# Kernel tuning notes

Hardware: AMD Instinct MI355X
Metric: run time of the kernel (lower is better)

## Reference

```python
import jax, jax.numpy as jnp
import numpy as np

BN_EPS = 1e-5

def conv_block(x, w, b, g, beta, m, v, a):
    # 1x1 conv (pointwise) + eval-mode BatchNorm2d + PReLU (single shared alpha)
    y = jnp.einsum('oc,bcft->boft', w, x) + b[None, :, None, None]
    scale = (g / jnp.sqrt(v + BN_EPS))[None, :, None, None]
    y = (y - m[None, :, None, None]) * scale + beta[None, :, None, None]
    return jnp.where(y >= 0, y, a * y)

def setup_inputs() -> dict:
    key = jax.random.key(0)
    ks = jax.random.split(key, 16)
    B, C, F, T = 4, 64, 128, 512
    d_c = C // 2
    inp = jax.random.normal(ks[0], (B, C, F, T), dtype=jnp.float32)
    # qkv projection Conv2Dblock params (1x1 conv c -> d_c)
    w1 = jax.random.normal(ks[1], (d_c, C), dtype=jnp.float32) * (1.0 / np.sqrt(C))
    b1 = jax.random.normal(ks[2], (d_c,), dtype=jnp.float32) * 0.01
    g1 = jnp.ones((d_c,), jnp.float32)
    be1 = jnp.zeros((d_c,), jnp.float32)
    m1 = jax.random.normal(ks[3], (d_c,), dtype=jnp.float32) * 0.01
    v1 = jax.random.uniform(ks[4], (d_c,), jnp.float32, 0.5, 1.5)
    a1 = jnp.asarray(0.25, jnp.float32)
    # output projection Conv2Dblock params (1x1 conv d_c -> c)
    wp = jax.random.normal(ks[5], (C, d_c), dtype=jnp.float32) * (1.0 / np.sqrt(d_c))
    bp = jax.random.normal(ks[6], (C,), dtype=jnp.float32) * 0.01
    g2 = jnp.ones((C,), jnp.float32)
    be2 = jnp.zeros((C,), jnp.float32)
    m2 = jax.random.normal(ks[7], (C,), dtype=jnp.float32) * 0.01
    v2 = jax.random.uniform(ks[8], (C,), jnp.float32, 0.5, 1.5)
    a2 = jnp.asarray(0.25, jnp.float32)
    return {"inp": inp, "w1": w1, "b1": b1, "g1": g1, "be1": be1, "m1": m1,
            "v1": v1, "a1": a1, "wp": wp, "bp": bp, "g2": g2, "be2": be2,
            "m2": m2, "v2": v2, "a2": a2}

def reference(inp, w1, b1, g1, be1, m1, v1, a1, wp, bp, g2, be2, m2, v2, a2):
    d_c = w1.shape[0]
    qkv = conv_block(inp, w1, b1, g1, be1, m1, v1, a1)           # [B, d_c, F, T]
    # per-frequency time attention scores, then recombine with values
    score = jnp.einsum('bcft,bcfy->bfty', qkv, qkv) / jnp.sqrt(jnp.asarray(d_c, qkv.dtype))
    score = jnp.einsum('bfty,bcfy->bcft', score, qkv)            # [B, d_c, F, T]
    # causal mask applied over the last two dims (F, T), as in the original
    Fd, Td = score.shape[-2], score.shape[-1]
    mask = (jnp.arange(Td)[None, :] - jnp.arange(Fd)[:, None]) >= (Td - Fd + 1)
    neg = -jnp.finfo(score.dtype).max
    score = jnp.where(mask[None, None, :, :], neg, score)
    score = jax.nn.softmax(score, axis=-1)
    score = conv_block(score, wp, bp, g2, be2, m2, v2, a2)       # [B, C, F, T]
    return score + inp
```

## Files before the change

### kernel.cpp

```cpp
#include <hip/hip_runtime.h>
#include <math.h>

#define Bv  4
#define Cv  64
#define DCv 32
#define Fv  128
#define Tv  512
#define FT  (Fv * 512)

__global__ __launch_bounds__(256, 4)
void kc1_conv(const float* __restrict__ inp,
              const float* __restrict__ w1, const float* __restrict__ b1,
              const float* __restrict__ g1, const float* __restrict__ be1,
              const float* __restrict__ m1, const float* __restrict__ v1,
              const float* __restrict__ a1,
              float* __restrict__ Qws)
{
    __shared__ __align__(16) float sW[Cv * DCv];
    __shared__ float sB[DCv];

    const int tid = threadIdx.x;
    const int bid = blockIdx.x;
    const int h   = bid & 1;
    const int bf  = bid >> 1;
    const int b   = bf >> 7;
    const int f   = bf & 127;

    #pragma unroll
    for (int i = 0; i < 8; ++i) {
        const int e = tid * 8 + i;
        const int c = e & 31, k = e >> 5;
        sW[e] = w1[c * Cv + k] * (g1[c] * rsqrtf(v1[c] + 1e-5f));
    }
    if (tid < DCv) {
        const float s = g1[tid] * rsqrtf(v1[tid] + 1e-5f);
        sB[tid] = (b1[tid] - m1[tid]) * s + be1[tid];
    }
    const float alpha1 = a1[0];
    __syncthreads();

    const int w  = tid >> 6, l = tid & 63;
    const int tl = l & 15, cl = l >> 4;
    const int r0 = cl * 8;
    const int t0 = h * 256 + w * 64 + tl * 4;

    const float* px = inp + (size_t)(b * Cv) * FT + f * 512 + t0;

    float acc[32];
    #pragma unroll
    for (int i = 0; i < 32; ++i) acc[i] = 0.f;

    #pragma unroll 8
    for (int k = 0; k < Cv; ++k) {
        const float4 x   = *(const float4*)&px[(size_t)k * FT];
        const float4 a0  = *(const float4*)&sW[k * DCv + r0];
        const float4 a1v = *(const float4*)&sW[k * DCv + r0 + 4];
        acc[0*4+0] = fmaf(a0.x, x.x, acc[0*4+0]); acc[0*4+1] = fmaf(a0.x, x.y, acc[0*4+1]);
        acc[0*4+2] = fmaf(a0.x, x.z, acc[0*4+2]); acc[0*4+3] = fmaf(a0.x, x.w, acc[0*4+3]);
        acc[1*4+0] = fmaf(a0.y, x.x, acc[1*4+0]); acc[1*4+1] = fmaf(a0.y, x.y, acc[1*4+1]);
        acc[1*4+2] = fmaf(a0.y, x.z, acc[1*4+2]); acc[1*4+3] = fmaf(a0.y, x.w, acc[1*4+3]);
        acc[2*4+0] = fmaf(a0.z, x.x, acc[2*4+0]); acc[2*4+1] = fmaf(a0.z, x.y, acc[2*4+1]);
        acc[2*4+2] = fmaf(a0.z, x.z, acc[2*4+2]); acc[2*4+3] = fmaf(a0.z, x.w, acc[2*4+3]);
        acc[3*4+0] = fmaf(a0.w, x.x, acc[3*4+0]); acc[3*4+1] = fmaf(a0.w, x.y, acc[3*4+1]);
        acc[3*4+2] = fmaf(a0.w, x.z, acc[3*4+2]); acc[3*4+3] = fmaf(a0.w, x.w, acc[3*4+3]);
        acc[4*4+0] = fmaf(a1v.x, x.x, acc[4*4+0]); acc[4*4+1] = fmaf(a1v.x, x.y, acc[4*4+1]);
        acc[4*4+2] = fmaf(a1v.x, x.z, acc[4*4+2]); acc[4*4+3] = fmaf(a1v.x, x.w, acc[4*4+3]);
        acc[5*4+0] = fmaf(a1v.y, x.x, acc[5*4+0]); acc[5*4+1] = fmaf(a1v.y, x.y, acc[5*4+1]);
        acc[5*4+2] = fmaf(a1v.y, x.z, acc[5*4+2]); acc[5*4+3] = fmaf(a1v.y, x.w, acc[5*4+3]);
        acc[6*4+0] = fmaf(a1v.z, x.x, acc[6*4+0]); acc[6*4+1] = fmaf(a1v.z, x.y, acc[6*4+1]);
        acc[6*4+2] = fmaf(a1v.z, x.z, acc[6*4+2]); acc[6*4+3] = fmaf(a1v.z, x.w, acc[6*4+3]);
        acc[7*4+0] = fmaf(a1v.w, x.x, acc[7*4+0]); acc[7*4+1] = fmaf(a1v.w, x.y, acc[7*4+1]);
        acc[7*4+2] = fmaf(a1v.w, x.z, acc[7*4+2]); acc[7*4+3] = fmaf(a1v.w, x.w, acc[7*4+3]);
    }

    const float b0 = sB[r0+0], b1_ = sB[r0+1], b2 = sB[r0+2], b3 = sB[r0+3];
    const float b4 = sB[r0+4], b5  = sB[r0+5], b6 = sB[r0+6], b7 = sB[r0+7];
    #pragma unroll
    for (int j = 0; j < 4; ++j) {
        float z0 = acc[0*4+j] + b0, z1 = acc[1*4+j] + b1_;
        float z2 = acc[2*4+j] + b2, z3 = acc[3*4+j] + b3;
        float z4 = acc[4*4+j] + b4, z5 = acc[5*4+j] + b5;
        float z6 = acc[6*4+j] + b6, z7 = acc[7*4+j] + b7;
        z0 = z0 >= 0.f ? z0 : alpha1 * z0;  z1 = z1 >= 0.f ? z1 : alpha1 * z1;
        z2 = z2 >= 0.f ? z2 : alpha1 * z2;  z3 = z3 >= 0.f ? z3 : alpha1 * z3;
        z4 = z4 >= 0.f ? z4 : alpha1 * z4;  z5 = z5 >= 0.f ? z5 : alpha1 * z5;
        z6 = z6 >= 0.f ? z6 : alpha1 * z6;  z7 = z7 >= 0.f ? z7 : alpha1 * z7;
        float4 v0; v0.x = z0; v0.y = z1; v0.z = z2; v0.w = z3;
        float4 v1; v1.x = z4; v1.y = z5; v1.z = z6; v1.w = z7;
        float* qg = Qws + ((size_t)bf * Tv + t0 + j) * DCv + r0;
        *(float4*)&qg[0] = v0;
        *(float4*)&qg[4] = v1;
    }
}

__global__ __launch_bounds__(256)
void km_build(const float* __restrict__ Qws, float* __restrict__ Mfull)
{
    __shared__ __align__(16) float sP[4][1024];

    const int tid   = threadIdx.x;
    const int bf    = blockIdx.x;
    const int slice = tid >> 6;
    const int l     = tid & 63;
    const int c1b   = l >> 3;
    const int c2b   = l & 7;

    const float* qp = Qws + ((size_t)bf * Tv + slice * 128) * DCv;
    float4 r0 = {0,0,0,0}, r1 = {0,0,0,0}, r2 = {0,0,0,0}, r3 = {0,0,0,0};
    #pragma unroll 4
    for (int i = 0; i < 128; ++i) {
        const float4 qa = *(const float4*)&qp[i * 32 + c1b * 4];
        const float4 qb = *(const float4*)&qp[i * 32 + c2b * 4];
        r0.x = fmaf(qa.x, qb.x, r0.x); r0.y = fmaf(qa.x, qb.y, r0.y);
        r0.z = fmaf(qa.x, qb.z, r0.z); r0.w = fmaf(qa.x, qb.w, r0.w);
        r1.x = fmaf(qa.y, qb.x, r1.x); r1.y = fmaf(qa.y, qb.y, r1.y);
        r1.z = fmaf(qa.y, qb.z, r1.z); r1.w = fmaf(qa.y, qb.w, r1.w);
        r2.x = fmaf(qa.z, qb.x, r2.x); r2.y = fmaf(qa.z, qb.y, r2.y);
        r2.z = fmaf(qa.z, qb.z, r2.z); r2.w = fmaf(qa.z, qb.w, r2.w);
        r3.x = fmaf(qa.w, qb.x, r3.x); r3.y = fmaf(qa.w, qb.y, r3.y);
        r3.z = fmaf(qa.w, qb.z, r3.z); r3.w = fmaf(qa.w, qb.w, r3.w);
    }
    *(float4*)&sP[slice][(c1b * 4 + 0) * DCv + c2b * 4] = r0;
    *(float4*)&sP[slice][(c1b * 4 + 1) * DCv + c2b * 4] = r1;
    *(float4*)&sP[slice][(c1b * 4 + 2) * DCv + c2b * 4] = r2;
    *(float4*)&sP[slice][(c1b * 4 + 3) * DCv + c2b * 4] = r3;
    __syncthreads();

    const float INV = 0.17677669529663687f;
    float4 v0 = *(const float4*)&sP[0][tid * 4];
    float4 v1 = *(const float4*)&sP[1][tid * 4];
    float4 v2 = *(const float4*)&sP[2][tid * 4];
    float4 v3 = *(const float4*)&sP[3][tid * 4];
    float4 o;
    o.x = ((v0.x + v1.x) + (v2.x + v3.x)) * INV;
    o.y = ((v0.y + v1.y) + (v2.y + v3.y)) * INV;
    o.z = ((v0.z + v1.z) + (v2.z + v3.z)) * INV;
    o.w = ((v0.w + v1.w) + (v2.w + v3.w)) * INV;
    *(float4*)&Mfull[(size_t)bf * 1024 + tid * 4] = o;
}

#define GEMM_CC(ACC, cc, a)                                       \
    ACC[(cc)*4+0] = fmaf(a.x, x0.x, ACC[(cc)*4+0]);               \
    ACC[(cc)*4+0] = fmaf(a.y, x1.x, ACC[(cc)*4+0]);               \
    ACC[(cc)*4+0] = fmaf(a.z, x2.x, ACC[(cc)*4+0]);               \
    ACC[(cc)*4+0] = fmaf(a.w, x3.x, ACC[(cc)*4+0]);               \
    ACC[(cc)*4+1] = fmaf(a.x, x0.y, ACC[(cc)*4+1]);               \
    ACC[(cc)*4+1] = fmaf(a.y, x1.y, ACC[(cc)*4+1]);               \
    ACC[(cc)*4+1] = fmaf(a.z, x2.y, ACC[(cc)*4+1]);               \
    ACC[(cc)*4+1] = fmaf(a.w, x3.y, ACC[(cc)*4+1]);               \
    ACC[(cc)*4+2] = fmaf(a.x, x0.z, ACC[(cc)*4+2]);               \
    ACC[(cc)*4+2] = fmaf(a.y, x1.z, ACC[(cc)*4+2]);               \
    ACC[(cc)*4+2] = fmaf(a.z, x2.z, ACC[(cc)*4+2]);               \
    ACC[(cc)*4+2] = fmaf(a.w, x3.z, ACC[(cc)*4+2]);               \
    ACC[(cc)*4+3] = fmaf(a.x, x0.w, ACC[(cc)*4+3]);               \
    ACC[(cc)*4+3] = fmaf(a.y, x1.w, ACC[(cc)*4+3]);               \
    ACC[(cc)*4+3] = fmaf(a.z, x2.w, ACC[(cc)*4+3]);               \
    ACC[(cc)*4+3] = fmaf(a.w, x3.w, ACC[(cc)*4+3]);

__global__ __launch_bounds__(512, 2)
void kf_fused(const float* __restrict__ inp,
              const float* __restrict__ Qws, const float* __restrict__ Mfull,
              const float* __restrict__ wp, const float* __restrict__ bp,
              const float* __restrict__ g2, const float* __restrict__ be2,
              const float* __restrict__ m2, const float* __restrict__ v2,
              const float* __restrict__ a2,
              float* __restrict__ out)
{
    __shared__ __align__(16) float sX[DCv * Tv];
    __shared__ __align__(16) float sM[DCv * 36];
    __shared__ __align__(16) float sW[Cv * 36];
    __shared__ float sPartM[8][DCv], sPartS[8][DCv];
    __shared__ float sMx[DCv], sRZ[DCv];
    __shared__ float sB2[Cv];

    const int tid = threadIdx.x;
    const int bf  = blockIdx.x;
    const int b   = bf >> 7;
    const int f   = bf & 127;
    const int w   = tid >> 6;
    const int l   = tid & 63;
    const int tl  = l & 15;
    const int cl  = l >> 4;
    const int t0  = w * 64 + tl * 4;
    const int limit = f + (Tv - Fv + 1);
    const float alpha2 = a2[0];

    const float* qg = Qws + ((size_t)bf * Tv + tid) * DCv;
    float4 q0 = *(const float4*)&qg[0],  q1 = *(const float4*)&qg[4];
    float4 q2 = *(const float4*)&qg[8],  q3 = *(const float4*)&qg[12];
    float4 q4 = *(const float4*)&qg[16], q5 = *(const float4*)&qg[20];
    float4 q6 = *(const float4*)&qg[24], q7 = *(const float4*)&qg[28];

    if (tid < 256) {
        const int c = tid >> 3, k0 = (tid & 7) << 2;
        float4 v = *(const float4*)&Mfull[(size_t)bf * 1024 + tid * 4];
        *(float4*)&sM[c * 36 + k0] = v;
    }
    {
        const int c = tid >> 3, k0 = (tid & 7) << 2;
        const float s = g2[c] * rsqrtf(v2[c] + 1e-5f);
        float4 v = *(const float4*)&wp[tid * 4];
        v.x *= s; v.y *= s; v.z *= s; v.w *= s;
        *(float4*)&sW[c * 36 + k0] = v;
    }
    if (tid < Cv) {
        const float s = g2[tid] * rsqrtf(v2[tid] + 1e-5f);
        sB2[tid] = (bp[tid] - m2[tid]) * s + be2[tid];
    }

    {
        const int t = tid;
        sX[ 0*Tv+t]=q0.x; sX[ 1*Tv+t]=q0.y; sX[ 2*Tv+t]=q0.z; sX[ 3*Tv+t]=q0.w;
        sX[ 4*Tv+t]=q1.x; sX[ 5*Tv+t]=q1.y; sX[ 6*Tv+t]=q1.z; sX[ 7*Tv+t]=q1.w;
        sX[ 8*Tv+t]=q2.x; sX[ 9*Tv+t]=q2.y; sX[10*Tv+t]=q2.z; sX[11*Tv+t]=q2.w;
        sX[12*Tv+t]=q3.x; sX[13*Tv+t]=q3.y; sX[14*Tv+t]=q3.z; sX[15*Tv+t]=q3.w;
        sX[16*Tv+t]=q4.x; sX[17*Tv+t]=q4.y; sX[18*Tv+t]=q4.z; sX[19*Tv+t]=q4.w;
        sX[20*Tv+t]=q5.x; sX[21*Tv+t]=q5.y; sX[22*Tv+t]=q5.z; sX[23*Tv+t]=q5.w;
        sX[24*Tv+t]=q6.x; sX[25*Tv+t]=q6.y; sX[26*Tv+t]=q6.z; sX[27*Tv+t]=q6.w;
        sX[28*Tv+t]=q7.x; sX[29*Tv+t]=q7.y; sX[30*Tv+t]=q7.z; sX[31*Tv+t]=q7.w;
    }
    __syncthreads();

    float oA[16], oB[16];
    #pragma unroll
    for (int i = 0; i < 16; ++i) { oA[i] = 0.f; oB[i] = 0.f; }
    const int cA = cl * 4;
    const int cB = 16 + cl * 4;
    #pragma unroll
    for (int k0 = 0; k0 < 32; k0 += 4) {
        const float4 x0 = *(const float4*)&sX[(k0+0)*Tv + t0];
        const float4 x1 = *(const float4*)&sX[(k0+1)*Tv + t0];
        const float4 x2 = *(const float4*)&sX[(k0+2)*Tv + t0];
        const float4 x3 = *(const float4*)&sX[(k0+3)*Tv + t0];
        { const float4 a = *(const float4*)&sM[(cA+0)*36 + k0]; GEMM_CC(oA,0,a) }
        { const float4 a = *(const float4*)&sM[(cA+1)*36 + k0]; GEMM_CC(oA,1,a) }
        { const float4 a = *(const float4*)&sM[(cA+2)*36 + k0]; GEMM_CC(oA,2,a) }
        { const float4 a = *(const float4*)&sM[(cA+3)*36 + k0]; GEMM_CC(oA,3,a) }
        { const float4 a = *(const float4*)&sM[(cB+0)*36 + k0]; GEMM_CC(oB,0,a) }
        { const float4 a = *(const float4*)&sM[(cB+1)*36 + k0]; GEMM_CC(oB,1,a) }
        { const float4 a = *(const float4*)&sM[(cB+2)*36 + k0]; GEMM_CC(oB,2,a) }
        { const float4 a = *(const float4*)&sM[(cB+3)*36 + k0]; GEMM_CC(oB,3,a) }
    }

    #pragma unroll
    for (int jt = 0; jt < 4; ++jt) {
        if (t0 + jt >= limit) {
            #pragma unroll
            for (int cc = 0; cc < 4; ++cc) { oA[cc*4+jt] = -INFINITY; oB[cc*4+jt] = -INFINITY; }
        }
    }

    float mwA[4], mwB[4];
    #pragma unroll
    for (int cc = 0; cc < 4; ++cc) {
        float mA = fmaxf(fmaxf(oA[cc*4+0], oA[cc*4+1]), fmaxf(oA[cc*4+2], oA[cc*4+3]));
        float mB = fmaxf(fmaxf(oB[cc*4+0], oB[cc*4+1]), fmaxf(oB[cc*4+2], oB[cc*4+3]));
        #pragma unroll
        for (int s = 1; s < 16; s <<= 1) {
            mA = fmaxf(mA, __shfl_xor(mA, s));
            mB = fmaxf(mB, __shfl_xor(mB, s));
        }
        mA = fmaxf(mA, -1e30f);
        mB = fmaxf(mB, -1e30f);
        float sA = 0.f, sB = 0.f;
        #pragma unroll
        for (int jt = 0; jt < 4; ++jt) {
            oA[cc*4+jt] = __expf(oA[cc*4+jt] - mA); sA += oA[cc*4+jt];
            oB[cc*4+jt] = __expf(oB[cc*4+jt] - mB); sB += oB[cc*4+jt];
        }
        #pragma unroll
        for (int s = 1; s < 16; s <<= 1) {
            sA += __shfl_xor(sA, s);
            sB += __shfl_xor(sB, s);
        }
        mwA[cc] = mA; mwB[cc] = mB;
        if (tl == 0) {
            sPartM[w][cA + cc] = mA; sPartS[w][cA + cc] = sA;
            sPartM[w][cB + cc] = mB; sPartS[w][cB + cc] = sB;
        }
    }
    __syncthreads();
    if (tid < DCv) {
        float m = sPartM[0][tid];
        #pragma unroll
        for (int ww = 1; ww < 8; ++ww) m = fmaxf(m, sPartM[ww][tid]);
        float Z = 0.f;
        #pragma unroll
        for (int ww = 0; ww < 8; ++ww) Z += sPartS[ww][tid] * __expf(sPartM[ww][tid] - m);
        sMx[tid] = m;
        sRZ[tid] = 1.f / Z;
    }
    __syncthreads();

    #pragma unroll
    for (int cc = 0; cc < 4; ++cc) {
        const float scA = __expf(mwA[cc] - sMx[cA + cc]) * sRZ[cA + cc];
        const float scB = __expf(mwB[cc] - sMx[cB + cc]) * sRZ[cB + cc];
        float4 pA, pB;
        pA.x = oA[cc*4+0]*scA; pA.y = oA[cc*4+1]*scA; pA.z = oA[cc*4+2]*scA; pA.w = oA[cc*4+3]*scA;
        pB.x = oB[cc*4+0]*scB; pB.y = oB[cc*4+1]*scB; pB.z = oB[cc*4+2]*scB; pB.w = oB[cc*4+3]*scB;
        *(float4*)&sX[(cA + cc)*Tv + t0] = pA;
        *(float4*)&sX[(cB + cc)*Tv + t0] = pB;
    }
    __syncthreads();

    #pragma unroll 1
    for (int it = 0; it < 2; ++it) {
        const int oc0 = it * 32 + cl * 8;

        float acc[32];
        #pragma unroll
        for (int i = 0; i < 32; ++i) acc[i] = 0.f;

        #pragma unroll
        for (int k0 = 0; k0 < 32; k0 += 4) {
            const float4 x0 = *(const float4*)&sX[(k0+0)*Tv + t0];
            const float4 x1 = *(const float4*)&sX[(k0+1)*Tv + t0];
            const float4 x2 = *(const float4*)&sX[(k0+2)*Tv + t0];
            const float4 x3 = *(const float4*)&sX[(k0+3)*Tv + t0];
            { const float4 a = *(const float4*)&sW[(oc0+0)*36 + k0]; GEMM_CC(acc,0,a) }
            { const float4 a = *(const float4*)&sW[(oc0+1)*36 + k0]; GEMM_CC(acc,1,a) }
            { const float4 a = *(const float4*)&sW[(oc0+2)*36 + k0]; GEMM_CC(acc,2,a) }
            { const float4 a = *(const float4*)&sW[(oc0+3)*36 + k0]; GEMM_CC(acc,3,a) }
            { const float4 a = *(const float4*)&sW[(oc0+4)*36 + k0]; GEMM_CC(acc,4,a) }
            { const float4 a = *(const float4*)&sW[(oc0+5)*36 + k0]; GEMM_CC(acc,5,a) }
            { const float4 a = *(const float4*)&sW[(oc0+6)*36 + k0]; GEMM_CC(acc,6,a) }
            { const float4 a = *(const float4*)&sW[(oc0+7)*36 + k0]; GEMM_CC(acc,7,a) }
        }

        const float* rp = inp + ((size_t)(b * Cv + oc0) * Fv + f) * Tv + t0;
        float*       po = out + ((size_t)(b * Cv + oc0) * Fv + f) * Tv + t0;
        #pragma unroll
        for (int r = 0; r < 8; ++r) {
            const float4 rv = *(const float4*)&rp[(size_t)r * FT];
            const float bb = sB2[oc0 + r];
            float z0 = acc[r*4+0] + bb, z1 = acc[r*4+1] + bb;
            float z2 = acc[r*4+2] + bb, z3 = acc[r*4+3] + bb;
            z0 = z0 >= 0.f ? z0 : alpha2 * z0;
            z1 = z1 >= 0.f ? z1 : alpha2 * z1;
            z2 = z2 >= 0.f ? z2 : alpha2 * z2;
            z3 = z3 >= 0.f ? z3 : alpha2 * z3;
            float4 o4; o4.x = z0 + rv.x; o4.y = z1 + rv.y;
            o4.z = z2 + rv.z; o4.w = z3 + rv.w;
            *(float4*)&po[(size_t)r * FT] = o4;
        }
    }
}

extern "C" void kernel_launch(void* const* d_in, const int* in_sizes, int n_in,
                              void* d_out, int out_size, void* d_ws, size_t ws_size,
                              hipStream_t stream) {
    const float* inp = (const float*)d_in[0];
    const float* w1  = (const float*)d_in[1];
    const float* b1  = (const float*)d_in[2];
    const float* g1  = (const float*)d_in[3];
    const float* be1 = (const float*)d_in[4];
    const float* m1  = (const float*)d_in[5];
    const float* v1  = (const float*)d_in[6];
    const float* a1  = (const float*)d_in[7];
    const float* wp  = (const float*)d_in[8];
    const float* bp  = (const float*)d_in[9];
    const float* g2  = (const float*)d_in[10];
    const float* be2 = (const float*)d_in[11];
    const float* m2  = (const float*)d_in[12];
    const float* v2  = (const float*)d_in[13];
    const float* a2  = (const float*)d_in[14];

    float* Qws   = (float*)d_ws;
    float* Mfull = Qws + (size_t)Bv * Fv * Tv * DCv;

    kc1_conv<<<dim3(Bv * Fv * 2), dim3(256), 0, stream>>>(
        inp, w1, b1, g1, be1, m1, v1, a1, Qws);
    km_build<<<dim3(Bv * Fv), dim3(256), 0, stream>>>(Qws, Mfull);
    kf_fused<<<dim3(Bv * Fv), dim3(512), 0, stream>>>(
        inp, Qws, Mfull, wp, bp, g2, be2, m2, v2, a2, (float*)d_out);
}
```

Baseline: 87.23 us.

## Use bf16 MFMA for output projection conv in fused kernel

Replaces the FP32 FMA GEMM of the output 1x1 conv (64x32 weights times 32x512 softmax tile) with bf16 MFMA 16x16x32 instructions. Both the softmax probabilities and the BN-folded weights are converted to bf16 and stored in padded transposed shared-memory layouts. The aim is to cut the ALU cost of the projection. In exchange it lowers precision, and the epilogue now does scalar strided global loads and stores (4 rows per lane) instead of float4 accesses.

```diff
diff --git a/kernel.cpp b/kernel.cpp
--- a/kernel.cpp
+++ b/kernel.cpp
@@ -7,6 +7,14 @@
 #define Fv  128
 #define Tv  512
 #define FT  (Fv * 512)
+
+typedef __attribute__((ext_vector_type(8))) short bf16x8;
+typedef __attribute__((ext_vector_type(4))) float f32x4;
+
+__device__ __forceinline__ unsigned f2bf(float x) {
+    unsigned u = __float_as_uint(x);
+    return (u + 0x7FFFu + ((u >> 16) & 1u)) >> 16;
+}
 
 __global__ __launch_bounds__(256, 4)
 void kc1_conv(const float* __restrict__ inp,
@@ -168,7 +176,7 @@
 {
     __shared__ __align__(16) float sX[DCv * Tv];
     __shared__ __align__(16) float sM[DCv * 36];
-    __shared__ __align__(16) float sW[Cv * 36];
+    __shared__ __align__(16) unsigned short sWb[Cv * 40];
     __shared__ float sPartM[8][DCv], sPartS[8][DCv];
     __shared__ float sMx[DCv], sRZ[DCv];
     __shared__ float sB2[Cv];
@@ -197,11 +205,14 @@
         *(float4*)&sM[c * 36 + k0] = v;
     }
     {
-        const int c = tid >> 3, k0 = (tid & 7) << 2;
-        const float s = g2[c] * rsqrtf(v2[c] + 1e-5f);
+        const int oc = tid >> 3, k0 = (tid & 7) << 2;
+        const float s = g2[oc] * rsqrtf(v2[oc] + 1e-5f);
         float4 v = *(const float4*)&wp[tid * 4];
-        v.x *= s; v.y *= s; v.z *= s; v.w *= s;
-        *(float4*)&sW[c * 36 + k0] = v;
+        unsigned short* d = &sWb[oc * 40 + k0];
+        d[0] = (unsigned short)f2bf(v.x * s);
+        d[1] = (unsigned short)f2bf(v.y * s);
+        d[2] = (unsigned short)f2bf(v.z * s);
+        d[3] = (unsigned short)f2bf(v.w * s);
     }
     if (tid < Cv) {
         const float s = g2[tid] * rsqrtf(v2[tid] + 1e-5f);
@@ -292,57 +303,55 @@
     }
     __syncthreads();
 
-    #pragma unroll
-    for (int cc = 0; cc < 4; ++cc) {
-        const float scA = __expf(mwA[cc] - sMx[cA + cc]) * sRZ[cA + cc];
-        const float scB = __expf(mwB[cc] - sMx[cB + cc]) * sRZ[cB + cc];
-        float4 pA, pB;
-        pA.x = oA[cc*4+0]*scA; pA.y = oA[cc*4+1]*scA; pA.z = oA[cc*4+2]*scA; pA.w = oA[cc*4+3]*scA;
-        pB.x = oB[cc*4+0]*scB; pB.y = oB[cc*4+1]*scB; pB.z = oB[cc*4+2]*scB; pB.w = oB[cc*4+3]*scB;
-        *(float4*)&sX[(cA + cc)*Tv + t0] = pA;
-        *(float4*)&sX[(cB + cc)*Tv + t0] = pB;
-    }
-    __syncthreads();
-
-    #pragma unroll 1
-    for (int it = 0; it < 2; ++it) {
-        const int oc0 = it * 32 + cl * 8;
-
-        float acc[32];
-        #pragma unroll
-        for (int i = 0; i < 32; ++i) acc[i] = 0.f;
-
-        #pragma unroll
-        for (int k0 = 0; k0 < 32; k0 += 4) {
-            const float4 x0 = *(const float4*)&sX[(k0+0)*Tv + t0];
-            const float4 x1 = *(const float4*)&sX[(k0+1)*Tv + t0];
-            const float4 x2 = *(const float4*)&sX[(k0+2)*Tv + t0];
-            const float4 x3 = *(const float4*)&sX[(k0+3)*Tv + t0];
-            { const float4 a = *(const float4*)&sW[(oc0+0)*36 + k0]; GEMM_CC(acc,0,a) }
-            { const float4 a = *(const float4*)&sW[(oc0+1)*36 + k0]; GEMM_CC(acc,1,a) }
-            { const float4 a = *(const float4*)&sW[(oc0+2)*36 + k0]; GEMM_CC(acc,2,a) }
-            { const float4 a = *(const float4*)&sW[(oc0+3)*36 + k0]; GEMM_CC(acc,3,a) }
-            { const float4 a = *(const float4*)&sW[(oc0+4)*36 + k0]; GEMM_CC(acc,4,a) }
-            { const float4 a = *(const float4*)&sW[(oc0+5)*36 + k0]; GEMM_CC(acc,5,a) }
-            { const float4 a = *(const float4*)&sW[(oc0+6)*36 + k0]; GEMM_CC(acc,6,a) }
-            { const float4 a = *(const float4*)&sW[(oc0+7)*36 + k0]; GEMM_CC(acc,7,a) }
-        }
-
-        const float* rp = inp + ((size_t)(b * Cv + oc0) * Fv + f) * Tv + t0;
-        float*       po = out + ((size_t)(b * Cv + oc0) * Fv + f) * Tv + t0;
-        #pragma unroll
-        for (int r = 0; r < 8; ++r) {
-            const float4 rv = *(const float4*)&rp[(size_t)r * FT];
-            const float bb = sB2[oc0 + r];
-            float z0 = acc[r*4+0] + bb, z1 = acc[r*4+1] + bb;
-            float z2 = acc[r*4+2] + bb, z3 = acc[r*4+3] + bb;
-            z0 = z0 >= 0.f ? z0 : alpha2 * z0;
-            z1 = z1 >= 0.f ? z1 : alpha2 * z1;
-            z2 = z2 >= 0.f ? z2 : alpha2 * z2;
-            z3 = z3 >= 0.f ? z3 : alpha2 * z3;
-            float4 o4; o4.x = z0 + rv.x; o4.y = z1 + rv.y;
-            o4.z = z2 + rv.z; o4.w = z3 + rv.w;
-            *(float4*)&po[(size_t)r * FT] = o4;
+    unsigned short* sPb = (unsigned short*)sX;
+    {
+        float scAv[4], scBv[4];
+        #pragma unroll
+        for (int cc = 0; cc < 4; ++cc) {
+            scAv[cc] = __expf(mwA[cc] - sMx[cA + cc]) * sRZ[cA + cc];
+            scBv[cc] = __expf(mwB[cc] - sMx[cB + cc]) * sRZ[cB + cc];
+        }
+        #pragma unroll
+        for (int jt = 0; jt < 4; ++jt) {
+            const int t = t0 + jt;
+            uint2 va, vb;
+            va.x = f2bf(oA[0*4+jt]*scAv[0]) | (f2bf(oA[1*4+jt]*scAv[1]) << 16);
+            va.y = f2bf(oA[2*4+jt]*scAv[2]) | (f2bf(oA[3*4+jt]*scAv[3]) << 16);
+            vb.x = f2bf(oB[0*4+jt]*scBv[0]) | (f2bf(oB[1*4+jt]*scBv[1]) << 16);
+            vb.y = f2bf(oB[2*4+jt]*scBv[2]) | (f2bf(oB[3*4+jt]*scBv[3]) << 16);
+            *(uint2*)&sPb[t * 40 + cA] = va;
+            *(uint2*)&sPb[t * 40 + cB] = vb;
+        }
+    }
+    __syncthreads();
+
+    {
+        const int lr = l & 15, lk = l >> 4;
+        bf16x8 afr[4];
+        #pragma unroll
+        for (int o = 0; o < 4; ++o)
+            afr[o] = *(bf16x8*)&sWb[(o * 16 + lr) * 40 + lk * 8];
+        const int rhi = lk * 4;
+
+        #pragma unroll
+        for (int tt = 0; tt < 4; ++tt) {
+            const int tbase = (w * 4 + tt) * 16;
+            const bf16x8 bfr = *(bf16x8*)&sPb[(tbase + lr) * 40 + lk * 8];
+            const int colg = tbase + lr;
+            #pragma unroll
+            for (int o = 0; o < 4; ++o) {
+                f32x4 d = {0.f, 0.f, 0.f, 0.f};
+                d = __builtin_amdgcn_mfma_f32_16x16x32_bf16(afr[o], bfr, d, 0, 0, 0);
+                const int ocr = o * 16 + rhi;
+                const float* rp = inp + ((size_t)(b * Cv + ocr) * Fv + f) * Tv + colg;
+                float*       po = out + ((size_t)(b * Cv + ocr) * Fv + f) * Tv + colg;
+                #pragma unroll
+                for (int r = 0; r < 4; ++r) {
+                    float z = d[r] + sB2[ocr + r];
+                    z = z >= 0.f ? z : alpha2 * z;
+                    po[(size_t)r * FT] = z + rp[(size_t)r * FT];
+                }
+            }
         }
     }
 }
```

After: 89.38 us. 2.5% more time.
